# Performance work log

Measured on AMD Instinct MI355X. Metric: run time of the kernel, lower is better.

Reference implementation:

```python
import jax, jax.numpy as jnp
import numpy as np

EPSILON = 5.0
B, D, C = 262144, 512, 1000


def setup_inputs() -> dict:
    key = jax.random.key(0)
    k1, k2, k3 = jax.random.split(key, 3)
    features = jax.random.normal(k1, (B, D), dtype=jnp.float32)
    means = jax.random.normal(k2, (C, D), dtype=jnp.float32)
    labels = jax.random.randint(k3, (B,), 0, C, dtype=jnp.int64)
    return {"features": features, "means": means, "labels": labels}


def reference(features, means, labels):
    # Gather per-sample class mean: [B, D]
    gathered = means[labels]
    diff = features - gathered
    # Per-sample L2 distance, then hinge clamp(epsilon - dist, min=0), mean over batch
    dist = jnp.sqrt(jnp.sum(diff * diff, axis=-1))  # [B]
    loss = jnp.mean(jnp.maximum(EPSILON - dist, 0.0))
    return loss
```

## Files before the change

kernel.cpp:

```cpp
#include <hip/hip_runtime.h>

#define EPSILON 5.0f

constexpr int BLOCKS  = 2048;
constexpr int THREADS = 256;

typedef float fx4 __attribute__((ext_vector_type(4)));

__global__ __launch_bounds__(THREADS) void ncl_partial_kernel(
    const float* __restrict__ features,
    const float* __restrict__ means,
    const int* __restrict__ labels,
    float* __restrict__ partials,
    int B)
{
    const int lane = threadIdx.x & 63;
    const int globalWave = blockIdx.x * (THREADS >> 6) + (threadIdx.x >> 6);
    const int totalWaves = gridDim.x * (THREADS >> 6);

    const fx4* __restrict__ F = reinterpret_cast<const fx4*>(features);
    const fx4* __restrict__ M = reinterpret_cast<const fx4*>(means);

    float wsum = 0.0f;

    int row = globalWave;
    int cls0 = (row < B) ? labels[row] : 0;
    {
        const int r1 = row + totalWaves;
        int cls1 = (r1 < B) ? labels[r1] : 0;

        fx4 f0 = {0,0,0,0}, f1 = {0,0,0,0}, m0 = {0,0,0,0}, m1 = {0,0,0,0};
        if (row < B) {
            const fx4* f = F + (size_t)row  * 128;
            const fx4* m = M + (size_t)cls0 * 128;
            f0 = __builtin_nontemporal_load(f + lane);
            f1 = __builtin_nontemporal_load(f + lane + 64);
            m0 = m[lane];
            m1 = m[lane + 64];
        }

        while (row < B) {
            const int nrow = row + totalWaves;

            fx4 nf0 = {0,0,0,0}, nf1 = {0,0,0,0}, nm0 = {0,0,0,0}, nm1 = {0,0,0,0};
            if (nrow < B) {
                const fx4* f = F + (size_t)nrow * 128;
                const fx4* m = M + (size_t)cls1 * 128;
                nf0 = __builtin_nontemporal_load(f + lane);
                nf1 = __builtin_nontemporal_load(f + lane + 64);
                nm0 = m[lane];
                nm1 = m[lane + 64];
            }
            const int r2   = row + 2 * totalWaves;
            const int cls2 = (r2 < B) ? labels[r2] : 0;

            fx4 d0 = f0 - m0;
            fx4 d1 = f1 - m1;
            float ax = d0.x * d0.x, ay = d0.y * d0.y,
                  az = d0.z * d0.z, aw = d0.w * d0.w;
            ax = fmaf(d1.x, d1.x, ax); ay = fmaf(d1.y, d1.y, ay);
            az = fmaf(d1.z, d1.z, az); aw = fmaf(d1.w, d1.w, aw);
            float acc = (ax + ay) + (az + aw);

            #pragma unroll
            for (int off = 32; off > 0; off >>= 1)
                acc += __shfl_xor(acc, off, 64);

            if (lane == 0)
                wsum += fmaxf(EPSILON - sqrtf(acc), 0.0f);

            f0 = nf0; f1 = nf1; m0 = nm0; m1 = nm1;
            cls1 = cls2;
            row  = nrow;
        }
    }

    __shared__ float s[THREADS >> 6];
    const int wv = threadIdx.x >> 6;
    if (lane == 0) s[wv] = wsum;
    __syncthreads();
    if (threadIdx.x == 0) {
        float t = 0.0f;
        #pragma unroll
        for (int i = 0; i < (THREADS >> 6); ++i) t += s[i];
        partials[blockIdx.x] = t;
    }
}

__global__ __launch_bounds__(THREADS) void ncl_final_kernel(
    const float* __restrict__ partials,
    int n,
    float* __restrict__ out,
    float invB)
{
    float t = 0.0f;
    for (int i = threadIdx.x; i < n; i += THREADS) t += partials[i];

    #pragma unroll
    for (int off = 32; off > 0; off >>= 1)
        t += __shfl_xor(t, off, 64);

    __shared__ float s[THREADS >> 6];
    const int lane = threadIdx.x & 63;
    const int wv   = threadIdx.x >> 6;
    if (lane == 0) s[wv] = t;
    __syncthreads();
    if (threadIdx.x == 0) {
        float acc = 0.0f;
        #pragma unroll
        for (int i = 0; i < (THREADS >> 6); ++i) acc += s[i];
        out[0] = acc * invB;
    }
}

extern "C" void kernel_launch(void* const* d_in, const int* in_sizes, int n_in,
                              void* d_out, int out_size, void* d_ws, size_t ws_size,
                              hipStream_t stream) {
    const float* features = (const float*)d_in[0];
    const float* means    = (const float*)d_in[1];
    const int*   labels   = (const int*)d_in[2];
    float* out = (float*)d_out;

    const int B = in_sizes[2];
    float* partials = (float*)d_ws;

    ncl_partial_kernel<<<BLOCKS, THREADS, 0, stream>>>(features, means, labels,
                                                       partials, B);
    ncl_final_kernel<<<1, THREADS, 0, stream>>>(partials, BLOCKS, out,
                                                1.0f / (float)B);
}
```

Baseline: 102.4 us.

## Process row pairs per wave and fuse final reduction via last-block atomic

Each wave now handles two rows per iteration, doubling the loads in flight and interleaving the two shuffle reductions. The separate final-reduction kernel is replaced by a last-block-done pattern using an atomic counter, with a memset added to reset the counter. This trades one kernel launch for a memset plus fences and atomics, and raises register pressure. Odd B would drop the last row, since only B/2 pairs are processed.

```diff
diff --git a/kernel.cpp b/kernel.cpp
--- a/kernel.cpp
+++ b/kernel.cpp
@@ -7,75 +7,104 @@
 
 typedef float fx4 __attribute__((ext_vector_type(4)));
 
-__global__ __launch_bounds__(THREADS) void ncl_partial_kernel(
+__global__ __launch_bounds__(THREADS) void ncl_fused_kernel(
     const float* __restrict__ features,
     const float* __restrict__ means,
     const int* __restrict__ labels,
     float* __restrict__ partials,
-    int B)
+    unsigned int* __restrict__ counter,
+    float* __restrict__ out,
+    int B, float invB)
 {
     const int lane = threadIdx.x & 63;
     const int globalWave = blockIdx.x * (THREADS >> 6) + (threadIdx.x >> 6);
     const int totalWaves = gridDim.x * (THREADS >> 6);
+    const int nPairs = B >> 1;
 
     const fx4* __restrict__ F = reinterpret_cast<const fx4*>(features);
     const fx4* __restrict__ M = reinterpret_cast<const fx4*>(means);
 
     float wsum = 0.0f;
 
-    int row = globalWave;
-    int cls0 = (row < B) ? labels[row] : 0;
+    int p = globalWave;
+    int clsA = 0, clsB = 0;
+    if (p < nPairs) { clsA = labels[2 * p]; clsB = labels[2 * p + 1]; }
+
+    fx4 fa0{0,0,0,0}, fa1{0,0,0,0}, ma0{0,0,0,0}, ma1{0,0,0,0};
+    fx4 fb0{0,0,0,0}, fb1{0,0,0,0}, mb0{0,0,0,0}, mb1{0,0,0,0};
+    if (p < nPairs) {
+        const fx4* fa = F + (size_t)(2 * p)     * 128;
+        const fx4* fb = F + (size_t)(2 * p + 1) * 128;
+        const fx4* ma = M + (size_t)clsA * 128;
+        const fx4* mb = M + (size_t)clsB * 128;
+        fa0 = __builtin_nontemporal_load(fa + lane);
+        fa1 = __builtin_nontemporal_load(fa + lane + 64);
+        fb0 = __builtin_nontemporal_load(fb + lane);
+        fb1 = __builtin_nontemporal_load(fb + lane + 64);
+        ma0 = ma[lane]; ma1 = ma[lane + 64];
+        mb0 = mb[lane]; mb1 = mb[lane + 64];
+    }
+    int nclsA = 0, nclsB = 0;
     {
-        const int r1 = row + totalWaves;
-        int cls1 = (r1 < B) ? labels[r1] : 0;
+        const int np = p + totalWaves;
+        if (np < nPairs) { nclsA = labels[2 * np]; nclsB = labels[2 * np + 1]; }
+    }
 
-        fx4 f0 = {0,0,0,0}, f1 = {0,0,0,0}, m0 = {0,0,0,0}, m1 = {0,0,0,0};
-        if (row < B) {
-            const fx4* f = F + (size_t)row  * 128;
-            const fx4* m = M + (size_t)cls0 * 128;
-            f0 = __builtin_nontemporal_load(f + lane);
-            f1 = __builtin_nontemporal_load(f + lane + 64);
-            m0 = m[lane];
-            m1 = m[lane + 64];
+    while (p < nPairs) {
+        const int np = p + totalWaves;
+
+        fx4 xfa0{0,0,0,0}, xfa1{0,0,0,0}, xma0{0,0,0,0}, xma1{0,0,0,0};
+        fx4 xfb0{0,0,0,0}, xfb1{0,0,0,0}, xmb0{0,0,0,0}, xmb1{0,0,0,0};
+        if (np < nPairs) {
+            const fx4* fa = F + (size_t)(2 * np)     * 128;
+            const fx4* fb = F + (size_t)(2 * np + 1) * 128;
+            const fx4* ma = M + (size_t)nclsA * 128;
+            const fx4* mb = M + (size_t)nclsB * 128;
+            xfa0 = __builtin_nontemporal_load(fa + lane);
+            xfa1 = __builtin_nontemporal_load(fa + lane + 64);
+            xfb0 = __builtin_nontemporal_load(fb + lane);
+            xfb1 = __builtin_nontemporal_load(fb + lane + 64);
+            xma0 = ma[lane]; xma1 = ma[lane + 64];
+            xmb0 = mb[lane]; xmb1 = mb[lane + 64];
+        }
+        int yclsA = 0, yclsB = 0;
+        {
+            const int pp = p + 2 * totalWaves;
+            if (pp < nPairs) { yclsA = labels[2 * pp]; yclsB = labels[2 * pp + 1]; }
         }
 
-        while (row < B) {
-            const int nrow = row + totalWaves;
+        fx4 da0 = fa0 - ma0, da1 = fa1 - ma1;
+        fx4 db0 = fb0 - mb0, db1 = fb1 - mb1;
+        float a0 = da0.x * da0.x, a1 = da0.y * da0.y,
+              a2 = da0.z * da0.z, a3 = da0.w * da0.w;
+        float b0 = db0.x * db0.x, b1 = db0.y * db0.y,
+              b2 = db0.z * db0.z, b3 = db0.w * db0.w;
+        a0 = fmaf(da1.x, da1.x, a0); a1 = fmaf(da1.y, da1.y, a1);
+        a2 = fmaf(da1.z, da1.z, a2); a3 = fmaf(da1.w, da1.w, a3);
+        b0 = fmaf(db1.x, db1.x, b0); b1 = fmaf(db1.y, db1.y, b1);
+        b2 = fmaf(db1.z, db1.z, b2); b3 = fmaf(db1.w, db1.w, b3);
+        float accA = (a0 + a1) + (a2 + a3);
+        float accB = (b0 + b1) + (b2 + b3);
 
-            fx4 nf0 = {0,0,0,0}, nf1 = {0,0,0,0}, nm0 = {0,0,0,0}, nm1 = {0,0,0,0};
-            if (nrow < B) {
-                const fx4* f = F + (size_t)nrow * 128;
-                const fx4* m = M + (size_t)cls1 * 128;
-                nf0 = __builtin_nontemporal_load(f + lane);
-                nf1 = __builtin_nontemporal_load(f + lane + 64);
-                nm0 = m[lane];
-                nm1 = m[lane + 64];
-            }
-            const int r2   = row + 2 * totalWaves;
-            const int cls2 = (r2 < B) ? labels[r2] : 0;
+        #pragma unroll
+        for (int off = 32; off > 0; off >>= 1) {
+            accA += __shfl_xor(accA, off, 64);
+            accB += __shfl_xor(accB, off, 64);
+        }
 
-            fx4 d0 = f0 - m0;
-            fx4 d1 = f1 - m1;
-            float ax = d0.x * d0.x, ay = d0.y * d0.y,
-                  az = d0.z * d0.z, aw = d0.w * d0.w;
-            ax = fmaf(d1.x, d1.x, ax); ay = fmaf(d1.y, d1.y, ay);
-            az = fmaf(d1.z, d1.z, az); aw = fmaf(d1.w, d1.w, aw);
-            float acc = (ax + ay) + (az + aw);
+        if (lane == 0) {
+            wsum += fmaxf(EPSILON - sqrtf(accA), 0.0f);
+            wsum += fmaxf(EPSILON - sqrtf(accB), 0.0f);
+        }
 
-            #pragma unroll
-            for (int off = 32; off > 0; off >>= 1)
-                acc += __shfl_xor(acc, off, 64);
-
-            if (lane == 0)
-                wsum += fmaxf(EPSILON - sqrtf(acc), 0.0f);
-
-            f0 = nf0; f1 = nf1; m0 = nm0; m1 = nm1;
-            cls1 = cls2;
-            row  = nrow;
-        }
+        fa0 = xfa0; fa1 = xfa1; ma0 = xma0; ma1 = xma1;
+        fb0 = xfb0; fb1 = xfb1; mb0 = xmb0; mb1 = xmb1;
+        nclsA = yclsA; nclsB = yclsB;
+        p = np;
     }
 
     __shared__ float s[THREADS >> 6];
+    __shared__ bool lastBlock;
     const int wv = threadIdx.x >> 6;
     if (lane == 0) s[wv] = wsum;
     __syncthreads();
@@ -84,32 +113,28 @@
         #pragma unroll
         for (int i = 0; i < (THREADS >> 6); ++i) t += s[i];
         partials[blockIdx.x] = t;
+        __threadfence();
+        const unsigned int prev = atomicAdd(counter, 1u);
+        lastBlock = (prev == (unsigned int)(gridDim.x - 1));
     }
-}
+    __syncthreads();
 
-__global__ __launch_bounds__(THREADS) void ncl_final_kernel(
-    const float* __restrict__ partials,
-    int n,
-    float* __restrict__ out,
-    float invB)
-{
-    float t = 0.0f;
-    for (int i = threadIdx.x; i < n; i += THREADS) t += partials[i];
-
-    #pragma unroll
-    for (int off = 32; off > 0; off >>= 1)
-        t += __shfl_xor(t, off, 64);
-
-    __shared__ float s[THREADS >> 6];
-    const int lane = threadIdx.x & 63;
-    const int wv   = threadIdx.x >> 6;
-    if (lane == 0) s[wv] = t;
-    __syncthreads();
-    if (threadIdx.x == 0) {
-        float acc = 0.0f;
+    if (lastBlock) {
+        __threadfence();
+        float t = 0.0f;
+        for (int i = threadIdx.x; i < (int)gridDim.x; i += THREADS)
+            t += partials[i];
         #pragma unroll
-        for (int i = 0; i < (THREADS >> 6); ++i) acc += s[i];
-        out[0] = acc * invB;
+        for (int off = 32; off > 0; off >>= 1)
+            t += __shfl_xor(t, off, 64);
+        if (lane == 0) s[wv] = t;
+        __syncthreads();
+        if (threadIdx.x == 0) {
+            float acc = 0.0f;
+            #pragma unroll
+            for (int i = 0; i < (THREADS >> 6); ++i) acc += s[i];
+            out[0] = acc * invB;
+        }
     }
 }
 
@@ -123,9 +148,11 @@
 
     const int B = in_sizes[2];
     float* partials = (float*)d_ws;
+    unsigned int* counter = (unsigned int*)((char*)d_ws + BLOCKS * sizeof(float));
 
-    ncl_partial_kernel<<<BLOCKS, THREADS, 0, stream>>>(features, means, labels,
-                                                       partials, B);
-    ncl_final_kernel<<<1, THREADS, 0, stream>>>(partials, BLOCKS, out,
-                                                1.0f / (float)B);
+    hipMemsetAsync(counter, 0, sizeof(unsigned int), stream);
+
+    ncl_fused_kernel<<<BLOCKS, THREADS, 0, stream>>>(features, means, labels,
+                                                     partials, counter, out,
+                                                     B, 1.0f / (float)B);
 }
```

After: 203.1 us. 98.3% more time.
